# Kernel optimization log

Measured on AMD Instinct MI355X. Metric: run time of the kernel, lower is better.

Reference implementation:

```python
import jax, jax.numpy as jnp
import numpy as np

D = 1024       # hidden_dim
H = 16         # n_heads
HD = D // H    # head dim = 64
V = 32000      # vocab_size
S = 4          # n_scales
IT = 6         # iters_per_scale
L = S * IT     # total_layers = 24 (one shared block, looped)
G = 16         # n_rot_groups
g = D // G     # group dim = 64
FF = 4 * D     # ff_mult * hidden_dim
N_TRI = g * (g - 1) // 2  # 2016 upper-tri skew params per group
EPS = 1e-6


def rmsnorm(x, w):
    return x * jax.lax.rsqrt(jnp.mean(x * x, axis=-1, keepdims=True) + EPS) * w


def setup_inputs() -> dict:
    key = jax.random.key(0)
    ks = jax.random.split(key, 12)
    rn = lambda k, shape, s: jax.random.normal(k, shape, jnp.float32) * s
    return {
        "tokens": jax.random.randint(ks[0], (1, 1024), 0, V),
        "embed_w": rn(ks[1], (V, D), 0.02),
        "lm_head_w": rn(ks[2], (V, D), 0.02),
        "norm_w": jnp.ones((D,), jnp.float32),
        "layer_gamma": 1.0 + rn(ks[3], (L, D), 0.02),
        "layer_beta": rn(ks[4], (L, D), 0.02),
        "iter_scale": 1.0 + rn(ks[5], (S, IT), 0.02),
        "skew_upper": rn(ks[6], (L, G, N_TRI), 0.02),
        "ln1_w": jnp.ones((D,), jnp.float32),
        "ln2_w": jnp.ones((D,), jnp.float32),
        "wqkv": rn(ks[7], (D, 3 * D), 0.02),
        "wo": rn(ks[8], (D, D), 0.02),
        "w1": rn(ks[9], (D, FF), 0.02),
        "w2": rn(ks[10], (FF, D), 0.02),
    }


def _rotations(skew_upper):
    """Cayley transform per layer/group: R = (I - A/2)^-1 (I + A/2), A skew-symm."""
    rows, cols = np.triu_indices(g, k=1)
    def one_layer(su):  # su: (G, N_TRI)
        A = jnp.zeros((G, g, g), su.dtype).at[:, rows, cols].set(su)
        A = A - jnp.swapaxes(A, -1, -2)
        I = jnp.eye(g, dtype=su.dtype)
        return jnp.linalg.solve(I - 0.5 * A, I + 0.5 * A)  # (G, g, g)
    return jax.vmap(one_layer)(skew_upper)  # (L, G, g, g)


def _block(x, gamma, beta, ln1_w, ln2_w, wqkv, wo, w1, w2):
    """Pre-norm causal transformer block with (gamma, beta) affine modulation."""
    B, T, _ = x.shape
    h = rmsnorm(x, ln1_w) * gamma + beta
    qkv = h @ wqkv  # (B, T, 3D)
    q, k, v = jnp.split(qkv, 3, axis=-1)
    q = q.reshape(B, T, H, HD)
    k = k.reshape(B, T, H, HD)
    v = v.reshape(B, T, H, HD)
    scores = jnp.einsum('bqhd,bkhd->bhqk', q, k) / np.sqrt(HD).astype(np.float32)
    causal = jnp.tril(jnp.ones((T, T), bool))
    scores = jnp.where(causal, scores, jnp.float32(-1e9))
    attn = jax.nn.softmax(scores, axis=-1)
    attn_out = jnp.einsum('bhqk,bkhd->bqhd', attn, v).reshape(B, T, D) @ wo
    x = x + attn_out
    x = x + jax.nn.gelu(rmsnorm(x, ln2_w) @ w1) @ w2
    return x


def reference(tokens, embed_w, lm_head_w, norm_w, layer_gamma, layer_beta,
              iter_scale, skew_upper, ln1_w, ln2_w, wqkv, wo, w1, w2):
    B, T = tokens.shape
    x = embed_w[tokens].astype(jnp.float32)  # (B, T, D)
    R = _rotations(skew_upper)               # (L, G, g, g)
    its = iter_scale.reshape(-1)             # (L,) scale index order matches loop
    for l in range(L):
        blk = _block(x, layer_gamma[l], layer_beta[l], ln1_w, ln2_w, wqkv, wo, w1, w2)
        x = x + (blk - x) * its[l]           # affine residual blend
        xg = x.reshape(B, T, G, g)
        x = jnp.einsum('btgi,gij->btgj', xg, R[l]).reshape(B, T, D)  # group rotation
    x = rmsnorm(x, norm_w)
    return x @ lm_head_w.T                   # (B, T, V) logits
```

## Files before the change

kernel.cpp:

```cpp
#include <hip/hip_runtime.h>
#include <hip/hip_bf16.h>
#include <math.h>

constexpr int kD = 1024;
constexpr int kH = 16;
constexpr int kV = 32000;
constexpr int kT = 1024;
constexpr int kG = 16;
constexpr int kFF = 4096;
constexpr int kL = 24;
constexpr int kNTRI = 2016;
#define EPSF 1e-6f
#define L2E 1.44269504088896f

typedef __bf16 bf16x8 __attribute__((ext_vector_type(8)));
typedef __bf16 bf16x4 __attribute__((ext_vector_type(4)));
typedef float f32x4 __attribute__((ext_vector_type(4)));

#define GLOAD16(g, l)                                                   \
  __builtin_amdgcn_global_load_lds(                                     \
      (const __attribute__((address_space(1))) void*)(g),               \
      (__attribute__((address_space(3))) void*)(l), 16, 0, 0)

__global__ __launch_bounds__(256) void cayley_kernel(const float* __restrict__ skew,
                                                     float* __restrict__ R) {
  int lg = blockIdx.x;
  int tid = threadIdx.x;
  int r = tid & 63, q = tid >> 6;
  __shared__ float Ms[64][65];
  __shared__ float Bs[64][65];
  const float* su = skew + (size_t)lg * kNTRI;
#pragma unroll
  for (int cc = 0; cc < 16; ++cc) {
    int c = q * 16 + cc;
    float a = 0.f;
    if (r < c) a = su[r * (127 - r) / 2 + (c - r - 1)];
    else if (r > c) a = -su[c * (127 - c) / 2 + (r - c - 1)];
    Ms[r][c] = (r == c ? 1.f : 0.f) - 0.5f * a;
    Bs[r][c] = (r == c ? 1.f : 0.f) + 0.5f * a;
  }
  __syncthreads();
  for (int k = 0; k < 64; ++k) {
    float ip = 1.f / Ms[k][k];
    float f = Ms[r][k];
    float beta = (r == k) ? (1.f - ip) : (f * ip);
    float mk[16], bk[16];
#pragma unroll
    for (int cc = 0; cc < 16; ++cc) {
      mk[cc] = Ms[k][q * 16 + cc];
      bk[cc] = Bs[k][q * 16 + cc];
    }
    __syncthreads();
#pragma unroll
    for (int cc = 0; cc < 16; ++cc) {
      int c = q * 16 + cc;
      Ms[r][c] -= beta * mk[cc];
      Bs[r][c] -= beta * bk[cc];
    }
    __syncthreads();
  }
  float* Ro = R + ((size_t)lg * 64 + r) * 64;
#pragma unroll
  for (int cc = 0; cc < 16; ++cc) Ro[q * 16 + cc] = Bs[r][q * 16 + cc];
}

__global__ __launch_bounds__(256) void embed_kernel(const int* __restrict__ tok,
                                                    const float* __restrict__ ew,
                                                    float* __restrict__ x) {
  int i = blockIdx.x * 256 + threadIdx.x;
  int t = i >> 8;
  int d4 = i & 255;
  int v = tok[t];
  reinterpret_cast<float4*>(x)[i] =
      reinterpret_cast<const float4*>(ew + (size_t)v * kD)[d4];
}

__global__ __launch_bounds__(256) void cast_kernel(const float* __restrict__ W,
                                                   __bf16* __restrict__ O) {
  size_t i = ((size_t)blockIdx.x * 256 + threadIdx.x) * 8;
  float4 f0 = *reinterpret_cast<const float4*>(W + i);
  float4 f1 = *reinterpret_cast<const float4*>(W + i + 4);
  bf16x8 v;
  v[0] = (__bf16)f0.x; v[1] = (__bf16)f0.y;
  v[2] = (__bf16)f0.z; v[3] = (__bf16)f0.w;
  v[4] = (__bf16)f1.x; v[5] = (__bf16)f1.y;
  v[6] = (__bf16)f1.z; v[7] = (__bf16)f1.w;
  *reinterpret_cast<bf16x8*>(O + i) = v;
}

__global__ __launch_bounds__(256) void convt_kernel(const float* __restrict__ W,
                                                    __bf16* __restrict__ WT,
                                                    int K, int N) {
  __shared__ float tile[64][65];
  int t = threadIdx.x;
  int n0 = blockIdx.x * 64, k0 = blockIdx.y * 64;
#pragma unroll
  for (int r = 0; r < 4; ++r) {
    int kr = r * 16 + (t >> 4);
    int nc = (t & 15) * 4;
    float4 v = *reinterpret_cast<const float4*>(&W[(size_t)(k0 + kr) * N + n0 + nc]);
    tile[kr][nc + 0] = v.x;
    tile[kr][nc + 1] = v.y;
    tile[kr][nc + 2] = v.z;
    tile[kr][nc + 3] = v.w;
  }
  __syncthreads();
#pragma unroll
  for (int r = 0; r < 2; ++r) {
    int idx = r * 256 + t;
    int nrow = idx >> 3, kc = (idx & 7) * 8;
    bf16x8 v;
#pragma unroll
    for (int j = 0; j < 8; ++j) v[j] = (__bf16)tile[kc + j][nrow];
    *reinterpret_cast<bf16x8*>(&WT[(size_t)(n0 + nrow) * K + k0 + kc]) = v;
  }
}

template <bool AFFINE>
__global__ __launch_bounds__(256) void rms_kernel(const float* __restrict__ x,
                                                  const float* __restrict__ w,
                                                  const float* __restrict__ gamma,
                                                  const float* __restrict__ beta,
                                                  __bf16* __restrict__ out) {
  int t = blockIdx.x, tid = threadIdx.x;
  __shared__ float red4[4];
  float4 xv = reinterpret_cast<const float4*>(x + (size_t)t * kD)[tid];
  float ss = xv.x * xv.x + xv.y * xv.y + xv.z * xv.z + xv.w * xv.w;
#pragma unroll
  for (int o = 1; o < 64; o <<= 1) ss += __shfl_xor(ss, o);
  if ((tid & 63) == 0) red4[tid >> 6] = ss;
  __syncthreads();
  float tot = red4[0] + red4[1] + red4[2] + red4[3];
  float rms = rsqrtf(tot / (float)kD + EPSF);
  float4 wv = reinterpret_cast<const float4*>(w)[tid];
  float o0 = xv.x * rms * wv.x;
  float o1 = xv.y * rms * wv.y;
  float o2 = xv.z * rms * wv.z;
  float o3 = xv.w * rms * wv.w;
  if (AFFINE) {
    float4 gv = reinterpret_cast<const float4*>(gamma)[tid];
    float4 bv = reinterpret_cast<const float4*>(beta)[tid];
    o0 = o0 * gv.x + bv.x;
    o1 = o1 * gv.y + bv.y;
    o2 = o2 * gv.z + bv.z;
    o3 = o3 * gv.w + bv.w;
  }
  bf16x4 ov;
  ov[0] = (__bf16)o0; ov[1] = (__bf16)o1; ov[2] = (__bf16)o2; ov[3] = (__bf16)o3;
  *reinterpret_cast<bf16x4*>(out + (size_t)t * kD + tid * 4) = ov;
}

__global__ __launch_bounds__(256) void rms_red_kernel(const float* __restrict__ x,
                                                      const float* __restrict__ p0,
                                                      const float* __restrict__ p1,
                                                      const float* __restrict__ w,
                                                      float* __restrict__ y,
                                                      __bf16* __restrict__ hb) {
  int t = blockIdx.x, tid = threadIdx.x;
  __shared__ float red4[4];
  size_t base = (size_t)t * kD;
  float4 xv = reinterpret_cast<const float4*>(x + base)[tid];
  float4 a = reinterpret_cast<const float4*>(p0 + base)[tid];
  float4 b = reinterpret_cast<const float4*>(p1 + base)[tid];
  float4 yv;
  yv.x = xv.x + a.x + b.x;
  yv.y = xv.y + a.y + b.y;
  yv.z = xv.z + a.z + b.z;
  yv.w = xv.w + a.w + b.w;
  reinterpret_cast<float4*>(y + base)[tid] = yv;
  float ss = yv.x * yv.x + yv.y * yv.y + yv.z * yv.z + yv.w * yv.w;
#pragma unroll
  for (int o = 1; o < 64; o <<= 1) ss += __shfl_xor(ss, o);
  if ((tid & 63) == 0) red4[tid >> 6] = ss;
  __syncthreads();
  float tot = red4[0] + red4[1] + red4[2] + red4[3];
  float rms = rsqrtf(tot / (float)kD + EPSF);
  float4 wv = reinterpret_cast<const float4*>(w)[tid];
  bf16x4 ov;
  ov[0] = (__bf16)(yv.x * rms * wv.x);
  ov[1] = (__bf16)(yv.y * rms * wv.y);
  ov[2] = (__bf16)(yv.z * rms * wv.z);
  ov[3] = (__bf16)(yv.w * rms * wv.w);
  *reinterpret_cast<bf16x4*>(hb + base + tid * 4) = ov;
}

template <int BM, int BN, int NW, int EPI, bool BF32, int KSPLIT = 1>
__global__ __launch_bounds__(NW * 64) void gemm_kernel(
    const __bf16* __restrict__ A, const void* __restrict__ Bv,
    const float* res, void* __restrict__ Cv, int M, int N, int K) {
  constexpr int WCOLS = (NW == 4) ? 2 : 4;
  constexpr int FM = (BM / 2) / 16;
  constexpr int FN = (BN / WCOLS) / 16;
  constexpr int AISS = BM / 8 / NW;
  constexpr int BISS = BN / 8 / NW;
  __shared__ __bf16 As[BM * 64];
  __shared__ __bf16 Bs[BN * 64];
  char* AsB = (char*)As;
  char* BsB = (char*)Bs;
  int tid = threadIdx.x;
  int w = tid >> 6, lane = tid & 63;
  int mt = M / BM, nt = N / BN;
  int cpx = gridDim.x >> 3;
  int id = (blockIdx.x & 7) * cpx + (blockIdx.x >> 3);
  int ks_id = id / (mt * nt);
  int rem = id % (mt * nt);
  int bm = (rem % mt) * BM, bn = (rem / mt) * BN;
  int kbeg = ks_id * (K / KSPLIT), kend = kbeg + K / KSPLIT;
  int lrow = lane & 15, g = lane >> 4;
  int grow = lane >> 3;
  int gswz = ((lane & 7) ^ grow) * 8;
  int rsw = (lrow & 7) << 4;
  int wm = (NW == 4) ? (w >> 1) : (w >> 2);
  int wn = (NW == 4) ? (w & 1) : (w & 3);
  int wr = wm * (BM / 2), wc = wn * (BN / WCOLS);
  f32x4 acc[FM][FN] = {};
  const __bf16* B16 = (const __bf16*)Bv;
  const float* B32 = (const float*)Bv;

  for (int k0 = kbeg; k0 < kend; k0 += 64) {
#pragma unroll
    for (int i = 0; i < AISS; ++i) {
      int rbase = (i * NW + w) * 8;
      GLOAD16(&A[(size_t)(bm + rbase + grow) * K + k0 + gswz], &As[rbase * 64]);
    }
    if (!BF32) {
#pragma unroll
      for (int i = 0; i < BISS; ++i) {
        int rbase = (i * NW + w) * 8;
        GLOAD16(&B16[(size_t)(bn + rbase + grow) * K + k0 + gswz], &Bs[rbase * 64]);
      }
    } else {
#pragma unroll
      for (int rrep = 0; rrep < BN * 8 / (NW * 64); ++rrep) {
        int cid = rrep * NW * 64 + tid;
        int row = cid >> 3, kc = (cid & 7) * 8;
        const float* src = &B32[(size_t)(bn + row) * K + k0 + kc];
        float4 f0 = *reinterpret_cast<const float4*>(src);
        float4 f1 = *reinterpret_cast<const float4*>(src + 4);
        bf16x8 v;
        v[0] = (__bf16)f0.x; v[1] = (__bf16)f0.y;
        v[2] = (__bf16)f0.z; v[3] = (__bf16)f0.w;
        v[4] = (__bf16)f1.x; v[5] = (__bf16)f1.y;
        v[6] = (__bf16)f1.z; v[7] = (__bf16)f1.w;
        int swc = ((cid & 7) ^ (row & 7)) * 16;
        *reinterpret_cast<bf16x8*>(BsB + row * 128 + swc) = v;
      }
    }
    __syncthreads();
#pragma unroll
    for (int ks = 0; ks < 2; ++ks) {
      bf16x8 af[FM], bg[FN];
#pragma unroll
      for (int i = 0; i < FM; ++i)
        af[i] = *reinterpret_cast<const bf16x8*>(
            AsB + (wr + i * 16 + lrow) * 128 + ((ks * 64 + g * 16) ^ rsw));
#pragma unroll
      for (int j = 0; j < FN; ++j)
        bg[j] = *reinterpret_cast<const bf16x8*>(
            BsB + (wc + j * 16 + lrow) * 128 + ((ks * 64 + g * 16) ^ rsw));
#pragma unroll
      for (int i = 0; i < FM; ++i)
#pragma unroll
        for (int j = 0; j < FN; ++j)
          acc[i][j] = __builtin_amdgcn_mfma_f32_16x16x32_bf16(af[i], bg[j],
                                                              acc[i][j], 0, 0, 0);
    }
    __syncthreads();
  }

  float* Cp = (float*)Cv + (size_t)ks_id * M * N;
  int crow0 = bm + wr + g * 4;
  int ccol0 = bn + wc + lrow;
#pragma unroll
  for (int i = 0; i < FM; ++i) {
#pragma unroll
    for (int j = 0; j < FN; ++j) {
#pragma unroll
      for (int r = 0; r < 4; ++r) {
        int row = crow0 + i * 16 + r;
        int col = ccol0 + j * 16;
        size_t idx = (size_t)row * N + col;
        float v = acc[i][j][r];
        if (EPI == 1) v += res[idx];
        if (EPI == 2) {
          float u = v;
          float z = 0.7978845608028654f * (u + 0.044715f * u * u * u);
          float ez = exp2f(z * (2.f * L2E));
          v = u * ez / (1.f + ez);
        }
        if (EPI == 2 || EPI == 3) ((__bf16*)Cv)[idx] = (__bf16)v;
        else Cp[idx] = v;
      }
    }
  }
}

__global__ __launch_bounds__(256) void fattn_kernel(const __bf16* __restrict__ qkv,
                                                    __bf16* __restrict__ out) {
  __shared__ __bf16 Ks[2][64 * 64];
  __shared__ __bf16 Vt[2][64 * 64];
  __shared__ __bf16 Ps[4 * 16 * 64];
  int tid = threadIdx.x;
  int bq = blockIdx.x * 64;
  int h = blockIdx.y;
  int w = tid >> 6, lane = tid & 63;
  int g = lane >> 4, lr = lane & 15;

  bf16x8 qf[2];
  const __bf16* qbase = qkv + (size_t)(bq + w * 16 + lr) * (3 * kD) + h * 64;
#pragma unroll
  for (int ks = 0; ks < 2; ++ks) {
    bf16x8 v = *reinterpret_cast<const bf16x8*>(qbase + ks * 32 + g * 8);
#pragma unroll
    for (int j = 0; j < 8; ++j) qf[ks][j] = (__bf16)((float)v[j] * 0.125f);
  }

  f32x4 acc[4] = {};
  float m = -1e30f, lsum = 0.f;

  int srow = tid >> 2, sseg = tid & 3;
  int vk = tid & 63, vd0 = (tid >> 6) * 16;
  char* PwB = (char*)(Ps + w * (16 * 64));
  int psw = (lr & 7) << 4;

  bf16x8 ka, kb2, va, vb;
  int ntiles = bq / 64 + 1;

  {
    const __bf16* src = qkv + (size_t)(srow) * (3 * kD) + kD + h * 64 + sseg * 16;
    ka = *reinterpret_cast<const bf16x8*>(src);
    kb2 = *reinterpret_cast<const bf16x8*>(src + 8);
    const __bf16* vsrc = qkv + (size_t)(vk) * (3 * kD) + 2 * kD + h * 64 + vd0;
    va = *reinterpret_cast<const bf16x8*>(vsrc);
    vb = *reinterpret_cast<const bf16x8*>(vsrc + 8);
    char* KsB = (char*)Ks[0];
    char* VtB = (char*)Vt[0];
    int bc = sseg * 32, sw = (srow & 7) << 4;
    *reinterpret_cast<bf16x8*>(KsB + srow * 128 + (bc ^ sw)) = ka;
    *reinterpret_cast<bf16x8*>(KsB + srow * 128 + ((bc + 16) ^ sw)) = kb2;
#pragma unroll
    for (int i = 0; i < 8; ++i) {
      int d = vd0 + i;
      *((__bf16*)(VtB + d * 128 + ((vk * 2) ^ ((d & 7) << 4)))) = va[i];
      d = vd0 + 8 + i;
      *((__bf16*)(VtB + d * 128 + ((vk * 2) ^ ((d & 7) << 4)))) = vb[i];
    }
  }

  int cur = 0;
  for (int kt = 0; kt < ntiles; ++kt) {
    if (kt + 1 < ntiles) {
      const __bf16* src =
          qkv + (size_t)((kt + 1) * 64 + srow) * (3 * kD) + kD + h * 64 + sseg * 16;
      ka = *reinterpret_cast<const bf16x8*>(src);
      kb2 = *reinterpret_cast<const bf16x8*>(src + 8);
      const __bf16* vsrc =
          qkv + (size_t)((kt + 1) * 64 + vk) * (3 * kD) + 2 * kD + h * 64 + vd0;
      va = *reinterpret_cast<const bf16x8*>(vsrc);
      vb = *reinterpret_cast<const bf16x8*>(vsrc + 8);
    }
    __syncthreads();

    char* KsB = (char*)Ks[cur];
    char* VtB = (char*)Vt[cur];
    bool diag = (kt == ntiles - 1);
    int jmax = diag ? w : 3;

    f32x4 s[4];
#pragma unroll
    for (int jj = 0; jj < 4; ++jj) {
      if (jj <= jmax) {
        int krow = jj * 16 + lr;
        int ksw = (lr & 7) << 4;
        bf16x8 k0 = *reinterpret_cast<const bf16x8*>(KsB + krow * 128 + ((g * 16) ^ ksw));
        bf16x8 k1 = *reinterpret_cast<const bf16x8*>(KsB + krow * 128 + ((64 + g * 16) ^ ksw));
        f32x4 z = {};
        z = __builtin_amdgcn_mfma_f32_16x16x32_bf16(k0, qf[0], z, 0, 0, 0);
        s[jj] = __builtin_amdgcn_mfma_f32_16x16x32_bf16(k1, qf[1], z, 0, 0, 0);
      } else {
        s[jj] = f32x4{-1e30f, -1e30f, -1e30f, -1e30f};
      }
    }
    if (diag) {
#pragma unroll
      for (int r = 0; r < 4; ++r)
        if (g * 4 + r > lr) s[w][r] = -1e30f;
    }

    float mt = -1e30f;
#pragma unroll
    for (int jj = 0; jj < 4; ++jj)
#pragma unroll
      for (int r = 0; r < 4; ++r) mt = fmaxf(mt, s[jj][r]);
    mt = fmaxf(mt, __shfl_xor(mt, 16));
    mt = fmaxf(mt, __shfl_xor(mt, 32));
    float mn = fmaxf(m, mt);
    float sc = exp2f((m - mn) * L2E);
    float p[4][4];
    float rs = 0.f;
#pragma unroll
    for (int jj = 0; jj < 4; ++jj)
#pragma unroll
      for (int r = 0; r < 4; ++r) {
        float e = exp2f((s[jj][r] - mn) * L2E);
        p[jj][r] = e;
        rs += e;
      }
    rs += __shfl_xor(rs, 16);
    rs += __shfl_xor(rs, 32);
    lsum = lsum * sc + rs;
    m = mn;
#pragma unroll
    for (int r = 0; r < 4; ++r) {
      float s4 = __shfl(sc, 20 * g + r);
#pragma unroll
      for (int dt = 0; dt < 4; ++dt) acc[dt][r] *= s4;
    }

#pragma unroll
    for (int jj = 0; jj < 4; ++jj) {
      bf16x4 pv;
#pragma unroll
      for (int r = 0; r < 4; ++r) pv[r] = (__bf16)p[jj][r];
      *reinterpret_cast<bf16x4*>(PwB + lr * 128 + ((jj * 32 + g * 8) ^ psw)) = pv;
    }

    {
      bf16x8 pa0 = *reinterpret_cast<const bf16x8*>(PwB + lr * 128 + ((g * 16) ^ psw));
      bf16x8 pa1 = *reinterpret_cast<const bf16x8*>(PwB + lr * 128 + ((64 + g * 16) ^ psw));
#pragma unroll
      for (int dt = 0; dt < 4; ++dt) {
        int vrow = dt * 16 + lr;
        int vsw = (lr & 7) << 4;
        bf16x8 vb0 = *reinterpret_cast<const bf16x8*>(VtB + vrow * 128 + ((g * 16) ^ vsw));
        bf16x8 vb1 = *reinterpret_cast<const bf16x8*>(VtB + vrow * 128 + ((64 + g * 16) ^ vsw));
        acc[dt] = __builtin_amdgcn_mfma_f32_16x16x32_bf16(pa0, vb0, acc[dt], 0, 0, 0);
        acc[dt] = __builtin_amdgcn_mfma_f32_16x16x32_bf16(pa1, vb1, acc[dt], 0, 0, 0);
      }
    }
    __syncthreads();

    if (kt + 1 < ntiles) {
      char* KsN = (char*)Ks[cur ^ 1];
      char* VtN = (char*)Vt[cur ^ 1];
      int bc = sseg * 32, sw = (srow & 7) << 4;
      *reinterpret_cast<bf16x8*>(KsN + srow * 128 + (bc ^ sw)) = ka;
      *reinterpret_cast<bf16x8*>(KsN + srow * 128 + ((bc + 16) ^ sw)) = kb2;
#pragma unroll
      for (int i = 0; i < 8; ++i) {
        int d = vd0 + i;
        *((__bf16*)(VtN + d * 128 + ((vk * 2) ^ ((d & 7) << 4)))) = va[i];
        d = vd0 + 8 + i;
        *((__bf16*)(VtN + d * 128 + ((vk * 2) ^ ((d & 7) << 4)))) = vb[i];
      }
      cur ^= 1;
    }
  }

  float linv = 1.f / lsum;
#pragma unroll
  for (int r = 0; r < 4; ++r) {
    float ir = __shfl(linv, 20 * g + r);
    int row = bq + w * 16 + g * 4 + r;
#pragma unroll
    for (int dt = 0; dt < 4; ++dt)
      out[(size_t)row * kD + h * 64 + dt * 16 + lr] = (__bf16)(acc[dt][r] * ir);
  }
}

__global__ __launch_bounds__(256) void blend_rot_kernel(const float* x,
                                                        const float* y,
                                                        const float* q0,
                                                        const float* q1,
                                                        const float* iscale,
                                                        int l,
                                                        const float* __restrict__ Rall,
                                                        float* xout) {
  int tc = blockIdx.x, gr = blockIdx.y;
  int tid = threadIdx.x;
  __shared__ float Rs[64 * 64];
  __shared__ float xb[64][65];
  float s = iscale[l];
  const float* Rg = Rall + ((size_t)l * kG + gr) * 4096;
  {
    int off = tid * 16;
#pragma unroll
    for (int q2 = 0; q2 < 4; ++q2) {
      float4 rv = *reinterpret_cast<const float4*>(Rg + off + q2 * 4);
      *reinterpret_cast<float4*>(&Rs[off + q2 * 4]) = rv;
    }
  }
  int tok = tid & 63, seg = (tid >> 6) * 16;
  {
    size_t base = (size_t)(tc * 64 + tok) * kD + gr * 64 + seg;
#pragma unroll
    for (int q2 = 0; q2 < 4; ++q2) {
      float4 xv = *reinterpret_cast<const float4*>(x + base + q2 * 4);
      float4 yv = *reinterpret_cast<const float4*>(y + base + q2 * 4);
      float4 a = *reinterpret_cast<const float4*>(q0 + base + q2 * 4);
      float4 b = *reinterpret_cast<const float4*>(q1 + base + q2 * 4);
      float y0 = yv.x + a.x + b.x;
      float y1 = yv.y + a.y + b.y;
      float y2 = yv.z + a.z + b.z;
      float y3 = yv.w + a.w + b.w;
      xb[tok][seg + q2 * 4 + 0] = xv.x + (y0 - xv.x) * s;
      xb[tok][seg + q2 * 4 + 1] = xv.y + (y1 - xv.y) * s;
      xb[tok][seg + q2 * 4 + 2] = xv.z + (y2 - xv.z) * s;
      xb[tok][seg + q2 * 4 + 3] = xv.w + (y3 - xv.w) * s;
    }
  }
  __syncthreads();
  float o[16] = {};
  for (int i = 0; i < 64; ++i) {
    float xv = xb[tok][i];
#pragma unroll
    for (int d = 0; d < 16; ++d) o[d] += xv * Rs[i * 64 + seg + d];
  }
  float* outr = xout + (size_t)(tc * 64 + tok) * kD + gr * 64 + seg;
#pragma unroll
  for (int q2 = 0; q2 < 4; ++q2) {
    float4 ov = {o[q2 * 4 + 0], o[q2 * 4 + 1], o[q2 * 4 + 2], o[q2 * 4 + 3]};
    *reinterpret_cast<float4*>(outr + q2 * 4) = ov;
  }
}

extern "C" void kernel_launch(void* const* d_in, const int* in_sizes, int n_in,
                              void* d_out, int out_size, void* d_ws, size_t ws_size,
                              hipStream_t stream) {
  const int* tokens = (const int*)d_in[0];
  const float* embed_w = (const float*)d_in[1];
  const float* lm_head_w = (const float*)d_in[2];
  const float* norm_w = (const float*)d_in[3];
  const float* layer_gamma = (const float*)d_in[4];
  const float* layer_beta = (const float*)d_in[5];
  const float* iter_scale = (const float*)d_in[6];
  const float* skew_upper = (const float*)d_in[7];
  const float* ln1_w = (const float*)d_in[8];
  const float* ln2_w = (const float*)d_in[9];
  const float* wqkv = (const float*)d_in[10];
  const float* wo = (const float*)d_in[11];
  const float* w1 = (const float*)d_in[12];
  const float* w2 = (const float*)d_in[13];
  float* out = (float*)d_out;

  float* x = (float*)d_ws;
  float* y = x + (size_t)kT * kD;
  __bf16* hb = (__bf16*)(y + (size_t)kT * kD);
  __bf16* ab = hb + (size_t)kT * kD;
  float* R = (float*)(ab + (size_t)kT * kD);
  __bf16* lmhb = (__bf16*)(R + (size_t)kL * kG * 4096);
  bool ws_big = ws_size >= (size_t)(4670464 + 16384000) * 4;

  __bf16* qkvb = (__bf16*)out;
  __bf16* ffb = (__bf16*)(out + 1572864);
  __bf16* wqkvT = (__bf16*)(out + 3670016);
  __bf16* woT = (__bf16*)(out + 5242880);
  __bf16* w1T = (__bf16*)(out + 5767168);
  __bf16* w2T = (__bf16*)(out + 7864320);
  float* wop = out + 9961472;
  float* w2p = out + 12058624;

  cayley_kernel<<<kL * kG, 256, 0, stream>>>(skew_upper, R);
  embed_kernel<<<kT * kD / 4 / 256, 256, 0, stream>>>(tokens, embed_w, x);
  convt_kernel<<<dim3(3 * kD / 64, kD / 64), 256, 0, stream>>>(wqkv, wqkvT, kD, 3 * kD);
  convt_kernel<<<dim3(kD / 64, kD / 64), 256, 0, stream>>>(wo, woT, kD, kD);
  convt_kernel<<<dim3(kFF / 64, kD / 64), 256, 0, stream>>>(w1, w1T, kD, kFF);
  convt_kernel<<<dim3(kD / 64, kFF / 64), 256, 0, stream>>>(w2, w2T, kFF, kD);
  if (ws_big)
    cast_kernel<<<kV * kD / 8 / 256, 256, 0, stream>>>(lm_head_w, lmhb);

  for (int l = 0; l < kL; ++l) {
    rms_kernel<true><<<kT, 256, 0, stream>>>(x, ln1_w, layer_gamma + (size_t)l * kD,
                                             layer_beta + (size_t)l * kD, hb);
    gemm_kernel<64, 128, 8, 3, false><<<(kT / 64) * (3 * kD / 128), 512, 0, stream>>>(
        hb, wqkvT, nullptr, qkvb, kT, 3 * kD, kD);
    fattn_kernel<<<dim3(kT / 64, kH), 256, 0, stream>>>(qkvb, ab);
    gemm_kernel<64, 64, 8, 0, false, 2><<<2 * (kT / 64) * (kD / 64), 512, 0, stream>>>(
        ab, woT, nullptr, wop, kT, kD, kD);
    rms_red_kernel<<<kT, 256, 0, stream>>>(x, wop, wop + (size_t)kT * kD, ln2_w, y, hb);
    gemm_kernel<64, 128, 8, 2, false><<<(kT / 64) * (kFF / 128), 512, 0, stream>>>(
        hb, w1T, nullptr, ffb, kT, kFF, kD);
    gemm_kernel<64, 64, 8, 0, false, 2><<<2 * (kT / 64) * (kD / 64), 512, 0, stream>>>(
        ffb, w2T, nullptr, w2p, kT, kD, kFF);
    blend_rot_kernel<<<dim3(kT / 64, kG), 256, 0, stream>>>(
        x, y, w2p, w2p + (size_t)kT * kD, iter_scale, l, R, x);
  }

  rms_kernel<false><<<kT, 256, 0, stream>>>(x, norm_w, nullptr, nullptr, hb);
  if (ws_big)
    gemm_kernel<256, 128, 8, 0, false><<<(kT / 256) * (kV / 128), 512, 0, stream>>>(
        hb, lmhb, nullptr, out, kT, kV, kD);
  else
    gemm_kernel<128, 128, 4, 0, true><<<(kT / 128) * (kV / 128), 256, 0, stream>>>(
        hb, lm_head_w, nullptr, out, kT, kV, kD);
}
```

Before: 2.651 ms.

## Double-buffer LDS tiles in per-layer GEMMs to overlap global loads with MFMA

Adds an optional double-buffered path to the GEMM kernel. It prefetches the next K-tile into a second LDS buffer with global_load_lds, then uses a partial vmcnt wait and raw s_barrier so the current tile's MFMAs overlap the next tile's loads. The path is enabled for the four per-layer GEMMs (QKV, Wo, W1, W2); the LM-head GEMM keeps the single-buffer path. LDS use doubles, which may lower occupancy, and the hand-written vmcnt counts must match the real number of outstanding loads to stay correct.

```diff
diff --git a/kernel.cpp b/kernel.cpp
--- a/kernel.cpp
+++ b/kernel.cpp
@@ -184,7 +184,7 @@
   *reinterpret_cast<bf16x4*>(hb + base + tid * 4) = ov;
 }
 
-template <int BM, int BN, int NW, int EPI, bool BF32, int KSPLIT = 1>
+template <int BM, int BN, int NW, int EPI, bool BF32, int KSPLIT = 1, bool DBUF = false>
 __global__ __launch_bounds__(NW * 64) void gemm_kernel(
     const __bf16* __restrict__ A, const void* __restrict__ Bv,
     const float* res, void* __restrict__ Cv, int M, int N, int K) {
@@ -193,8 +193,9 @@
   constexpr int FN = (BN / WCOLS) / 16;
   constexpr int AISS = BM / 8 / NW;
   constexpr int BISS = BN / 8 / NW;
-  __shared__ __bf16 As[BM * 64];
-  __shared__ __bf16 Bs[BN * 64];
+  constexpr int NI = AISS + BISS;
+  __shared__ __bf16 As[(DBUF ? 2 : 1) * BM * 64];
+  __shared__ __bf16 Bs[(DBUF ? 2 : 1) * BN * 64];
   char* AsB = (char*)As;
   char* BsB = (char*)Bs;
   int tid = threadIdx.x;
@@ -217,47 +218,34 @@
   const __bf16* B16 = (const __bf16*)Bv;
   const float* B32 = (const float*)Bv;
 
-  for (int k0 = kbeg; k0 < kend; k0 += 64) {
+  auto stage = [&](int buf, int k0) {
 #pragma unroll
     for (int i = 0; i < AISS; ++i) {
       int rbase = (i * NW + w) * 8;
-      GLOAD16(&A[(size_t)(bm + rbase + grow) * K + k0 + gswz], &As[rbase * 64]);
-    }
-    if (!BF32) {
-#pragma unroll
-      for (int i = 0; i < BISS; ++i) {
-        int rbase = (i * NW + w) * 8;
-        GLOAD16(&B16[(size_t)(bn + rbase + grow) * K + k0 + gswz], &Bs[rbase * 64]);
-      }
-    } else {
-#pragma unroll
-      for (int rrep = 0; rrep < BN * 8 / (NW * 64); ++rrep) {
-        int cid = rrep * NW * 64 + tid;
-        int row = cid >> 3, kc = (cid & 7) * 8;
-        const float* src = &B32[(size_t)(bn + row) * K + k0 + kc];
-        float4 f0 = *reinterpret_cast<const float4*>(src);
-        float4 f1 = *reinterpret_cast<const float4*>(src + 4);
-        bf16x8 v;
-        v[0] = (__bf16)f0.x; v[1] = (__bf16)f0.y;
-        v[2] = (__bf16)f0.z; v[3] = (__bf16)f0.w;
-        v[4] = (__bf16)f1.x; v[5] = (__bf16)f1.y;
-        v[6] = (__bf16)f1.z; v[7] = (__bf16)f1.w;
-        int swc = ((cid & 7) ^ (row & 7)) * 16;
-        *reinterpret_cast<bf16x8*>(BsB + row * 128 + swc) = v;
-      }
-    }
-    __syncthreads();
+      GLOAD16(&A[(size_t)(bm + rbase + grow) * K + k0 + gswz],
+              &As[buf * BM * 64 + rbase * 64]);
+    }
+#pragma unroll
+    for (int i = 0; i < BISS; ++i) {
+      int rbase = (i * NW + w) * 8;
+      GLOAD16(&B16[(size_t)(bn + rbase + grow) * K + k0 + gswz],
+              &Bs[buf * BN * 64 + rbase * 64]);
+    }
+  };
+
+  auto compute = [&](int buf) {
+    int offA = buf * BM * 128, offB = buf * BN * 128;
 #pragma unroll
     for (int ks = 0; ks < 2; ++ks) {
       bf16x8 af[FM], bg[FN];
 #pragma unroll
       for (int i = 0; i < FM; ++i)
         af[i] = *reinterpret_cast<const bf16x8*>(
-            AsB + (wr + i * 16 + lrow) * 128 + ((ks * 64 + g * 16) ^ rsw));
+            AsB + offA + (wr + i * 16 + lrow) * 128 + ((ks * 64 + g * 16) ^ rsw));
 #pragma unroll
       for (int j = 0; j < FN; ++j)
         bg[j] = *reinterpret_cast<const bf16x8*>(
-            BsB + (wc + j * 16 + lrow) * 128 + ((ks * 64 + g * 16) ^ rsw));
+            BsB + offB + (wc + j * 16 + lrow) * 128 + ((ks * 64 + g * 16) ^ rsw));
 #pragma unroll
       for (int i = 0; i < FM; ++i)
 #pragma unroll
@@ -265,7 +253,59 @@
           acc[i][j] = __builtin_amdgcn_mfma_f32_16x16x32_bf16(af[i], bg[j],
                                                               acc[i][j], 0, 0, 0);
     }
-    __syncthreads();
+  };
+
+  if constexpr (DBUF && !BF32) {
+    stage(0, kbeg);
+    int cur = 0;
+    for (int k0 = kbeg; k0 < kend; k0 += 64) {
+      bool more = (k0 + 64 < kend);
+      if (more) stage(cur ^ 1, k0 + 64);
+      if (more) {
+        if constexpr (NI == 2) asm volatile("s_waitcnt vmcnt(2)" ::: "memory");
+        else if constexpr (NI == 3) asm volatile("s_waitcnt vmcnt(3)" ::: "memory");
+        else if constexpr (NI == 4) asm volatile("s_waitcnt vmcnt(4)" ::: "memory");
+        else if constexpr (NI == 6) asm volatile("s_waitcnt vmcnt(6)" ::: "memory");
+        else asm volatile("s_waitcnt vmcnt(0)" ::: "memory");
+      } else {
+        asm volatile("s_waitcnt vmcnt(0)" ::: "memory");
+      }
+      __builtin_amdgcn_sched_barrier(0);
+      __builtin_amdgcn_s_barrier();
+      compute(cur);
+      __builtin_amdgcn_s_barrier();
+      cur ^= 1;
+    }
+  } else {
+    for (int k0 = kbeg; k0 < kend; k0 += 64) {
+      if (!BF32) {
+        stage(0, k0);
+      } else {
+#pragma unroll
+        for (int rrep = 0; rrep < BN * 8 / (NW * 64); ++rrep) {
+          int cid = rrep * NW * 64 + tid;
+          int row = cid >> 3, kc = (cid & 7) * 8;
+          const float* src = &B32[(size_t)(bn + row) * K + k0 + kc];
+          float4 f0 = *reinterpret_cast<const float4*>(src);
+          float4 f1 = *reinterpret_cast<const float4*>(src + 4);
+          bf16x8 v;
+          v[0] = (__bf16)f0.x; v[1] = (__bf16)f0.y;
+          v[2] = (__bf16)f0.z; v[3] = (__bf16)f0.w;
+          v[4] = (__bf16)f1.x; v[5] = (__bf16)f1.y;
+          v[6] = (__bf16)f1.z; v[7] = (__bf16)f1.w;
+          int swc = ((cid & 7) ^ (row & 7)) * 16;
+          *reinterpret_cast<bf16x8*>(BsB + row * 128 + swc) = v;
+        }
+#pragma unroll
+        for (int i = 0; i < AISS; ++i) {
+          int rbase = (i * NW + w) * 8;
+          GLOAD16(&A[(size_t)(bm + rbase + grow) * K + k0 + gswz], &As[rbase * 64]);
+        }
+      }
+      __syncthreads();
+      compute(0);
+      __syncthreads();
+    }
   }
 
   float* Cp = (float*)Cv + (size_t)ks_id * M * N;
@@ -572,15 +612,19 @@
   for (int l = 0; l < kL; ++l) {
     rms_kernel<true><<<kT, 256, 0, stream>>>(x, ln1_w, layer_gamma + (size_t)l * kD,
                                              layer_beta + (size_t)l * kD, hb);
-    gemm_kernel<64, 128, 8, 3, false><<<(kT / 64) * (3 * kD / 128), 512, 0, stream>>>(
+    gemm_kernel<64, 128, 8, 3, false, 1, true>
+        <<<(kT / 64) * (3 * kD / 128), 512, 0, stream>>>(
         hb, wqkvT, nullptr, qkvb, kT, 3 * kD, kD);
     fattn_kernel<<<dim3(kT / 64, kH), 256, 0, stream>>>(qkvb, ab);
-    gemm_kernel<64, 64, 8, 0, false, 2><<<2 * (kT / 64) * (kD / 64), 512, 0, stream>>>(
+    gemm_kernel<64, 64, 8, 0, false, 2, true>
+        <<<2 * (kT / 64) * (kD / 64), 512, 0, stream>>>(
         ab, woT, nullptr, wop, kT, kD, kD);
     rms_red_kernel<<<kT, 256, 0, stream>>>(x, wop, wop + (size_t)kT * kD, ln2_w, y, hb);
-    gemm_kernel<64, 128, 8, 2, false><<<(kT / 64) * (kFF / 128), 512, 0, stream>>>(
+    gemm_kernel<64, 128, 8, 2, false, 1, true>
+        <<<(kT / 64) * (kFF / 128), 512, 0, stream>>>(
         hb, w1T, nullptr, ffb, kT, kFF, kD);
-    gemm_kernel<64, 64, 8, 0, false, 2><<<2 * (kT / 64) * (kD / 64), 512, 0, stream>>>(
+    gemm_kernel<64, 64, 8, 0, false, 2, true>
+        <<<2 * (kT / 64) * (kD / 64), 512, 0, stream>>>(
         ffb, w2T, nullptr, w2p, kT, kD, kFF);
     blend_rot_kernel<<<dim3(kT / 64, kG), 256, 0, stream>>>(
         x, y, w2p, w2p + (size_t)kT * kD, iter_scale, l, R, x);
```

Measured after the change: 2.578 ms. 1.03x faster.
